# Kernel optimization log

Hardware: AMD Instinct MI355X
Metric: run time of the kernel (lower is better)

The kernel has to match this reference:

```python
import jax, jax.numpy as jnp
import numpy as np

N = 50000      # nodes
E = 600000     # edges
F_IN = 128     # num_node_features
H = 128        # hidden_channels
C = 10         # num_classes
G = 128        # graphs in batch


def setup_inputs() -> dict:
    key = jax.random.key(0)
    ks = jax.random.split(key, 12)
    x = jax.random.normal(ks[0], (N, F_IN), dtype=jnp.float32)
    edge_index = jax.random.randint(ks[1], (2, E), 0, N, dtype=jnp.int64)
    batch = jnp.sort(jax.random.randint(ks[2], (N,), 0, G, dtype=jnp.int64))
    s = 0.05
    return {
        "x": x,
        "W1": jax.random.normal(ks[3], (F_IN, H), jnp.float32) * s,
        "b1": jnp.zeros((H,), jnp.float32),
        "W2": jax.random.normal(ks[4], (H, H), jnp.float32) * s,
        "b2": jnp.zeros((H,), jnp.float32),
        "W3": jax.random.normal(ks[5], (H, H), jnp.float32) * s,
        "b3": jnp.zeros((H,), jnp.float32),
        "Wl": jax.random.normal(ks[6], (H, C), jnp.float32) * s,
        "bl": jnp.zeros((C,), jnp.float32),
        "edge_index": edge_index,
        "batch": batch,
    }


def _gcn_conv(h, W, b, src, dst, norm, n):
    # h: [N, din] -> linear (no bias), gather, scale, scatter-add, + bias
    h = h @ W                                  # [N, dout]
    msg = norm[:, None] * h[src]               # [E+N, dout]
    out = jax.ops.segment_sum(msg, dst, num_segments=n)
    return out + b


def reference(x, W1, b1, W2, b2, W3, b3, Wl, bl, edge_index, batch):
    n = x.shape[0]
    # add self-loops (PyG GCNConv default) and symmetric normalization
    loop = jnp.arange(n, dtype=edge_index.dtype)
    src = jnp.concatenate([edge_index[0], loop])   # [E+N]
    dst = jnp.concatenate([edge_index[1], loop])   # [E+N]
    deg = jax.ops.segment_sum(jnp.ones_like(dst, dtype=x.dtype), dst, num_segments=n)
    dinv = jnp.where(deg > 0, jax.lax.rsqrt(deg), 0.0)
    norm = dinv[src] * dinv[dst]                   # [E+N]

    h = jax.nn.relu(_gcn_conv(x, W1, b1, src, dst, norm, n))
    h = jax.nn.relu(_gcn_conv(h, W2, b2, src, dst, norm, n))
    h = jax.nn.relu(_gcn_conv(h, W3, b3, src, dst, norm, n))

    # global mean pool over graph ids
    sums = jax.ops.segment_sum(h, batch, num_segments=G)           # [G, H]
    cnts = jax.ops.segment_sum(jnp.ones((n,), h.dtype), batch, num_segments=G)
    pooled = sums / jnp.maximum(cnts, 1.0)[:, None]

    # dropout is identity at inference; final linear classifier
    return pooled @ Wl + bl                                        # [G, C]
```

## Files before the change

### kernel.cpp

```cpp
#include <hip/hip_runtime.h>

#define HID 128
#define CLS 10
#define RCAP 64

typedef short short8 __attribute__((ext_vector_type(8)));
typedef float f32x4 __attribute__((ext_vector_type(4)));

__device__ __forceinline__ unsigned short f2bf(float f) {
  union { float f; unsigned u; } v; v.f = f;
  unsigned u = v.u;
  return (unsigned short)((u + 0x7FFFu + ((u >> 16) & 1u)) >> 16);
}
__device__ __forceinline__ float bf_lo(unsigned p) { return __uint_as_float(p << 16); }
__device__ __forceinline__ float bf_hi(unsigned p) { return __uint_as_float(p & 0xFFFF0000u); }


__global__ __launch_bounds__(256) void zero_wt(int* __restrict__ degi, int n, int nbN,
                                               float* __restrict__ pooled, int gh,
                                               const float* __restrict__ W1,
                                               const float* __restrict__ W2,
                                               const float* __restrict__ W3,
                                               unsigned short* __restrict__ Wt) {
  int b = blockIdx.x;
  if (b < nbN) {
    int i = b * 256 + threadIdx.x;
    if (i < n) degi[i] = 0;
    if (i < gh) pooled[i] = 0.f;
    return;
  }
  int wb = b - nbN;
  int mat = wb >> 4;
  int part = wb & 15;
  const float* W = (mat == 0) ? W1 : (mat == 1) ? W2 : W3;
  unsigned short* o = Wt + (size_t)mat * HID * HID;
  int base = part * (HID * HID / 16);
  for (int r = 0; r < HID * HID / 16; r += 256) {
    int idx = base + r + threadIdx.x;
    int k = idx >> 7, nn = idx & 127;
    o[nn * HID + k] = f2bf(W[idx]);
  }
}

__global__ __launch_bounds__(256) void degree_k(const int* __restrict__ dst,
                                                int* __restrict__ degi,
                                                int* __restrict__ eslot, int E) {
  int e = blockIdx.x * 256 + threadIdx.x;
  if (e < E) eslot[e] = atomicAdd(&degi[dst[e]], 1);
}

__global__ __launch_bounds__(256) void csr_fill(const int* __restrict__ src,
                                                const int* __restrict__ dst,
                                                const int* __restrict__ eslot,
                                                int* __restrict__ col_src, int E) {
  int e = blockIdx.x * 256 + threadIdx.x;
  if (e >= E) return;
  int slot = eslot[e];
  if (slot < RCAP) col_src[(size_t)dst[e] * RCAP + slot] = src[e];
}


#define WTP 136

__global__ __launch_bounds__(256) void gemm_mfma(const void* __restrict__ Aptr,
                                                 int a_fp32,
                                                 const unsigned short* __restrict__ Wt,
                                                 const int* __restrict__ degi,
                                                 unsigned short* __restrict__ Tb,
                                                 int nrows) {
  __shared__ unsigned short sW[HID][WTP];
  int tid = threadIdx.x;
  int wave = tid >> 6, lane = tid & 63;
  int m_lo = lane & 15, quad = lane >> 4;
  int row0 = blockIdx.x * 128;
  int rbase = row0 + wave * 32;

  uint4 araw[2][4];
#pragma unroll
  for (int tr = 0; tr < 2; ++tr) {
    int grow = rbase + tr * 16 + m_lo;
    int gr = (grow < nrows) ? grow : (nrows - 1);
    if (a_fp32) {
      const float* Arow = (const float*)Aptr + (size_t)gr * HID;
#pragma unroll
      for (int kb = 0; kb < 4; ++kb) {
        float4 f0 = *(const float4*)&Arow[kb * 32 + quad * 8];
        float4 f1 = *(const float4*)&Arow[kb * 32 + quad * 8 + 4];
        uint4 u;
        u.x = (unsigned)f2bf(f0.x) | ((unsigned)f2bf(f0.y) << 16);
        u.y = (unsigned)f2bf(f0.z) | ((unsigned)f2bf(f0.w) << 16);
        u.z = (unsigned)f2bf(f1.x) | ((unsigned)f2bf(f1.y) << 16);
        u.w = (unsigned)f2bf(f1.z) | ((unsigned)f2bf(f1.w) << 16);
        araw[tr][kb] = u;
      }
    } else {
      const uint4* Arow = (const uint4*)((const unsigned*)Aptr + (size_t)gr * 64);
#pragma unroll
      for (int kb = 0; kb < 4; ++kb) araw[tr][kb] = Arow[kb * 4 + quad];
    }
  }

  const uint4* Wt4 = (const uint4*)Wt;
#pragma unroll
  for (int i = 0; i < 8; ++i) {
    int idx = i * 256 + tid;
    *(uint4*)&sW[idx >> 4][(idx & 15) * 8] = Wt4[idx];
  }
  __syncthreads();

  f32x4 acc[2][8];
#pragma unroll
  for (int tr = 0; tr < 2; ++tr)
#pragma unroll
    for (int tc = 0; tc < 8; ++tc) acc[tr][tc] = (f32x4)(0.f);

#pragma unroll
  for (int kb = 0; kb < 4; ++kb) {
    short8 b[8];
#pragma unroll
    for (int tc = 0; tc < 8; ++tc) {
      union { uint4 u; short8 s; } cv;
      cv.u = *(const uint4*)&sW[tc * 16 + m_lo][kb * 32 + quad * 8];
      b[tc] = cv.s;
    }
#pragma unroll
    for (int tr = 0; tr < 2; ++tr) {
      union { uint4 u; short8 s; } av;
      av.u = araw[tr][kb];
#pragma unroll
      for (int tc = 0; tc < 8; ++tc)
        acc[tr][tc] = __builtin_amdgcn_mfma_f32_16x16x32_bf16(av.s, b[tc], acc[tr][tc], 0, 0, 0);
    }
  }

#pragma unroll
  for (int tr = 0; tr < 2; ++tr) {
#pragma unroll
    for (int r = 0; r < 4; ++r) {
      int grow = rbase + tr * 16 + quad * 4 + r;
      if (grow < nrows) {
        float s = rsqrtf((float)degi[grow] + 1.0f);
        unsigned short* orow = &Tb[(size_t)grow * HID];
#pragma unroll
        for (int tc = 0; tc < 8; ++tc)
          orow[tc * 16 + m_lo] = f2bf(s * acc[tr][tc][r]);
      }
    }
  }
}


__global__ __launch_bounds__(256) void aggregate(const unsigned* __restrict__ Tb2,
                                                 const int* __restrict__ degi,
                                                 const int* __restrict__ col_src,
                                                 const float* __restrict__ bias,
                                                 unsigned* __restrict__ Hb, int n) {
  int w = (blockIdx.x * 256 + threadIdx.x) >> 6;
  int lane = threadIdx.x & 63;
  int sub = lane >> 4;
  int l4 = lane & 15;
  int node = w * 4 + sub;
  if (node >= n) return;

  uint4 sv = *(const uint4*)&Tb2[(size_t)node * 64 + l4 * 4];
  float a0 = bf_lo(sv.x), a1 = bf_hi(sv.x), a2 = bf_lo(sv.y), a3 = bf_hi(sv.y);
  float a4 = bf_lo(sv.z), a5 = bf_hi(sv.z), a6 = bf_lo(sv.w), a7 = bf_hi(sv.w);
  int deg = degi[node];
  const int* row = &col_src[(size_t)node * RCAP];
  int j = 0;
  for (; j + 8 <= deg; j += 8) {
    int idx[8];
#pragma unroll
    for (int u = 0; u < 8; ++u) idx[u] = row[j + u];
    uint4 v[8];
#pragma unroll
    for (int u = 0; u < 8; ++u) v[u] = *(const uint4*)&Tb2[(size_t)idx[u] * 64 + l4 * 4];
#pragma unroll
    for (int u = 0; u < 8; ++u) {
      a0 += bf_lo(v[u].x); a1 += bf_hi(v[u].x);
      a2 += bf_lo(v[u].y); a3 += bf_hi(v[u].y);
      a4 += bf_lo(v[u].z); a5 += bf_hi(v[u].z);
      a6 += bf_lo(v[u].w); a7 += bf_hi(v[u].w);
    }
  }
  if (j + 4 <= deg) {
    int idx[4];
#pragma unroll
    for (int u = 0; u < 4; ++u) idx[u] = row[j + u];
    uint4 v[4];
#pragma unroll
    for (int u = 0; u < 4; ++u) v[u] = *(const uint4*)&Tb2[(size_t)idx[u] * 64 + l4 * 4];
#pragma unroll
    for (int u = 0; u < 4; ++u) {
      a0 += bf_lo(v[u].x); a1 += bf_hi(v[u].x);
      a2 += bf_lo(v[u].y); a3 += bf_hi(v[u].y);
      a4 += bf_lo(v[u].z); a5 += bf_hi(v[u].z);
      a6 += bf_lo(v[u].w); a7 += bf_hi(v[u].w);
    }
    j += 4;
  }
  for (; j < deg; ++j) {
    uint4 v = *(const uint4*)&Tb2[(size_t)row[j] * 64 + l4 * 4];
    a0 += bf_lo(v.x); a1 += bf_hi(v.x);
    a2 += bf_lo(v.y); a3 += bf_hi(v.y);
    a4 += bf_lo(v.z); a5 += bf_hi(v.z);
    a6 += bf_lo(v.w); a7 += bf_hi(v.w);
  }
  float di = rsqrtf((float)deg + 1.0f);
  float4 bs0 = *(const float4*)&bias[l4 * 8];
  float4 bs1 = *(const float4*)&bias[l4 * 8 + 4];
  a0 = fmaxf(di * a0 + bs0.x, 0.f);
  a1 = fmaxf(di * a1 + bs0.y, 0.f);
  a2 = fmaxf(di * a2 + bs0.z, 0.f);
  a3 = fmaxf(di * a3 + bs0.w, 0.f);
  a4 = fmaxf(di * a4 + bs1.x, 0.f);
  a5 = fmaxf(di * a5 + bs1.y, 0.f);
  a6 = fmaxf(di * a6 + bs1.z, 0.f);
  a7 = fmaxf(di * a7 + bs1.w, 0.f);
  uint4 o;
  o.x = (unsigned)f2bf(a0) | ((unsigned)f2bf(a1) << 16);
  o.y = (unsigned)f2bf(a2) | ((unsigned)f2bf(a3) << 16);
  o.z = (unsigned)f2bf(a4) | ((unsigned)f2bf(a5) << 16);
  o.w = (unsigned)f2bf(a6) | ((unsigned)f2bf(a7) << 16);
  *(uint4*)&Hb[(size_t)node * 64 + l4 * 4] = o;
}


__global__ __launch_bounds__(64) void pool_partial(const unsigned* __restrict__ Hb,
                                                   const int* __restrict__ batch,
                                                   float* __restrict__ pooled, int n) {
  int t = threadIdx.x;
  int s = blockIdx.x * 16;
  if (s >= n) return;
  int e = min(s + 16, n);
  int g = batch[s];
  float ax = 0.f, ay = 0.f;
  for (int i = s; i < e; ++i) {
    int bi = batch[i];
    if (bi != g) {
      atomicAdd(&pooled[g * HID + 2 * t], ax);
      atomicAdd(&pooled[g * HID + 2 * t + 1], ay);
      ax = ay = 0.f;
      g = bi;
    }
    unsigned v = Hb[(size_t)i * 64 + t];
    ax += bf_lo(v);
    ay += bf_hi(v);
  }
  atomicAdd(&pooled[g * HID + 2 * t], ax);
  atomicAdd(&pooled[g * HID + 2 * t + 1], ay);
}

__global__ __launch_bounds__(128) void classify_k(const float* __restrict__ pooled,
                                                  const int* __restrict__ batch,
                                                  const float* __restrict__ Wl,
                                                  const float* __restrict__ bl,
                                                  float* __restrict__ out, int n) {
  int g = blockIdx.x;
  int t = threadIdx.x;
  int lo = 0, hi = n;
  while (lo < hi) { int mid = (lo + hi) >> 1; if (batch[mid] < g) lo = mid + 1; else hi = mid; }
  int s = lo;
  hi = n;
  while (lo < hi) { int mid = (lo + hi) >> 1; if (batch[mid] < g + 1) lo = mid + 1; else hi = mid; }
  float c = fmaxf((float)(lo - s), 1.0f);
  __shared__ float p[HID];
  p[t] = pooled[g * HID + t] / c;
  __syncthreads();
  if (t < CLS) {
    float o = bl[t];
    for (int j = 0; j < HID; ++j) o += p[j] * Wl[j * CLS + t];
    out[g * CLS + t] = o;
  }
}


extern "C" void kernel_launch(void* const* d_in, const int* in_sizes, int n_in,
                              void* d_out, int out_size, void* d_ws, size_t ws_size,
                              hipStream_t stream) {
  const float* x  = (const float*)d_in[0];
  const float* W1 = (const float*)d_in[1];
  const float* b1 = (const float*)d_in[2];
  const float* W2 = (const float*)d_in[3];
  const float* b2 = (const float*)d_in[4];
  const float* W3 = (const float*)d_in[5];
  const float* b3 = (const float*)d_in[6];
  const float* Wl = (const float*)d_in[7];
  const float* bl = (const float*)d_in[8];
  const int* edge_index = (const int*)d_in[9];
  const int* batch = (const int*)d_in[10];

  const int N = in_sizes[10];
  const int E = in_sizes[9] / 2;
  const int G = out_size / CLS;
  const int* src = edge_index;
  const int* dst = edge_index + E;

  uintptr_t p = (uintptr_t)d_ws;
  auto take = [&](size_t bytes) -> void* {
    void* r = (void*)p;
    p += (bytes + 255) & ~(size_t)255;
    return r;
  };
  int*      degi      = (int*)take((size_t)N * 4);
  int*      eslot     = (int*)take((size_t)E * 4);
  int*      col_src   = (int*)take((size_t)N * RCAP * 4);
  unsigned short* WtA = (unsigned short*)take((size_t)3 * HID * HID * 2);
  unsigned short* bufTb = (unsigned short*)take((size_t)N * HID * 2);
  unsigned* bufHb     = (unsigned*)take((size_t)N * 64 * 4);
  float*    pooled    = (float*)take((size_t)G * HID * 4);

  int nbN = (N + 255) / 256;
  int nbE = (E + 255) / 256;

  zero_wt<<<nbN + 48, 256, 0, stream>>>(degi, N, nbN, pooled, G * HID, W1, W2, W3, WtA);
  degree_k<<<nbE, 256, 0, stream>>>(dst, degi, eslot, E);
  csr_fill<<<nbE, 256, 0, stream>>>(src, dst, eslot, col_src, E);

  int gemmBlocks = (N + 127) / 128;
  int waves = (N + 3) / 4;
  int aggBlocks = (waves + 3) / 4;

  gemm_mfma<<<gemmBlocks, 256, 0, stream>>>(x, 1, WtA, degi, bufTb, N);
  aggregate<<<aggBlocks, 256, 0, stream>>>((unsigned*)bufTb, degi, col_src, b1, bufHb, N);
  gemm_mfma<<<gemmBlocks, 256, 0, stream>>>(bufHb, 0, WtA + (size_t)HID * HID, degi, bufTb, N);
  aggregate<<<aggBlocks, 256, 0, stream>>>((unsigned*)bufTb, degi, col_src, b2, bufHb, N);
  gemm_mfma<<<gemmBlocks, 256, 0, stream>>>(bufHb, 0, WtA + (size_t)2 * HID * HID, degi, bufTb, N);
  aggregate<<<aggBlocks, 256, 0, stream>>>((unsigned*)bufTb, degi, col_src, b3, bufHb, N);

  pool_partial<<<(N + 15) / 16, 64, 0, stream>>>(bufHb, batch, pooled, N);
  classify_k<<<G, 128, 0, stream>>>(pooled, batch, Wl, bl, (float*)d_out, N);
}
```

Before: 261.1 us.

## Fuse degree/CSR fill kernels and fuse last aggregation with mean-pool

Merges the degree-count and CSR-fill kernels into one pass that writes the column index right after the atomic slot reservation, dropping the eslot buffer and one launch. Fuses the final layer's aggregation with global pooling: each block aggregates 16 nodes into shared memory and then reduces per graph with atomics, skipping the bf16 write and re-read of the last hidden layer. The pooled sums now use fp32 activations instead of bf16-rounded ones, which slightly changes numerics.

```diff
diff --git a/kernel.cpp b/kernel.cpp
--- a/kernel.cpp
+++ b/kernel.cpp
@@ -42,21 +42,15 @@
   }
 }
 
-__global__ __launch_bounds__(256) void degree_k(const int* __restrict__ dst,
-                                                int* __restrict__ degi,
-                                                int* __restrict__ eslot, int E) {
-  int e = blockIdx.x * 256 + threadIdx.x;
-  if (e < E) eslot[e] = atomicAdd(&degi[dst[e]], 1);
-}
-
-__global__ __launch_bounds__(256) void csr_fill(const int* __restrict__ src,
-                                                const int* __restrict__ dst,
-                                                const int* __restrict__ eslot,
-                                                int* __restrict__ col_src, int E) {
+__global__ __launch_bounds__(256) void degree_fill(const int* __restrict__ src,
+                                                   const int* __restrict__ dst,
+                                                   int* __restrict__ degi,
+                                                   int* __restrict__ col_src, int E) {
   int e = blockIdx.x * 256 + threadIdx.x;
   if (e >= E) return;
-  int slot = eslot[e];
-  if (slot < RCAP) col_src[(size_t)dst[e] * RCAP + slot] = src[e];
+  int d = dst[e];
+  int slot = atomicAdd(&degi[d], 1);
+  if (slot < RCAP) col_src[(size_t)d * RCAP + slot] = src[e];
 }
 
 
@@ -150,6 +144,68 @@
 }
 
 
+__device__ __forceinline__ void agg_node(const unsigned* __restrict__ Tb2,
+                                         const int* __restrict__ degi,
+                                         const int* __restrict__ col_src,
+                                         const float* __restrict__ bias,
+                                         int node, int l4, float a[8]) {
+  uint4 sv = *(const uint4*)&Tb2[(size_t)node * 64 + l4 * 4];
+  a[0] = bf_lo(sv.x); a[1] = bf_hi(sv.x); a[2] = bf_lo(sv.y); a[3] = bf_hi(sv.y);
+  a[4] = bf_lo(sv.z); a[5] = bf_hi(sv.z); a[6] = bf_lo(sv.w); a[7] = bf_hi(sv.w);
+  int deg = degi[node];
+  const int* row = &col_src[(size_t)node * RCAP];
+  int j = 0;
+  for (; j + 8 <= deg; j += 8) {
+    int idx[8];
+#pragma unroll
+    for (int u = 0; u < 8; ++u) idx[u] = row[j + u];
+    uint4 v[8];
+#pragma unroll
+    for (int u = 0; u < 8; ++u) v[u] = *(const uint4*)&Tb2[(size_t)idx[u] * 64 + l4 * 4];
+#pragma unroll
+    for (int u = 0; u < 8; ++u) {
+      a[0] += bf_lo(v[u].x); a[1] += bf_hi(v[u].x);
+      a[2] += bf_lo(v[u].y); a[3] += bf_hi(v[u].y);
+      a[4] += bf_lo(v[u].z); a[5] += bf_hi(v[u].z);
+      a[6] += bf_lo(v[u].w); a[7] += bf_hi(v[u].w);
+    }
+  }
+  if (j + 4 <= deg) {
+    int idx[4];
+#pragma unroll
+    for (int u = 0; u < 4; ++u) idx[u] = row[j + u];
+    uint4 v[4];
+#pragma unroll
+    for (int u = 0; u < 4; ++u) v[u] = *(const uint4*)&Tb2[(size_t)idx[u] * 64 + l4 * 4];
+#pragma unroll
+    for (int u = 0; u < 4; ++u) {
+      a[0] += bf_lo(v[u].x); a[1] += bf_hi(v[u].x);
+      a[2] += bf_lo(v[u].y); a[3] += bf_hi(v[u].y);
+      a[4] += bf_lo(v[u].z); a[5] += bf_hi(v[u].z);
+      a[6] += bf_lo(v[u].w); a[7] += bf_hi(v[u].w);
+    }
+    j += 4;
+  }
+  for (; j < deg; ++j) {
+    uint4 v = *(const uint4*)&Tb2[(size_t)row[j] * 64 + l4 * 4];
+    a[0] += bf_lo(v.x); a[1] += bf_hi(v.x);
+    a[2] += bf_lo(v.y); a[3] += bf_hi(v.y);
+    a[4] += bf_lo(v.z); a[5] += bf_hi(v.z);
+    a[6] += bf_lo(v.w); a[7] += bf_hi(v.w);
+  }
+  float di = rsqrtf((float)deg + 1.0f);
+  float4 bs0 = *(const float4*)&bias[l4 * 8];
+  float4 bs1 = *(const float4*)&bias[l4 * 8 + 4];
+  a[0] = fmaxf(di * a[0] + bs0.x, 0.f);
+  a[1] = fmaxf(di * a[1] + bs0.y, 0.f);
+  a[2] = fmaxf(di * a[2] + bs0.z, 0.f);
+  a[3] = fmaxf(di * a[3] + bs0.w, 0.f);
+  a[4] = fmaxf(di * a[4] + bs1.x, 0.f);
+  a[5] = fmaxf(di * a[5] + bs1.y, 0.f);
+  a[6] = fmaxf(di * a[6] + bs1.z, 0.f);
+  a[7] = fmaxf(di * a[7] + bs1.w, 0.f);
+}
+
 __global__ __launch_bounds__(256) void aggregate(const unsigned* __restrict__ Tb2,
                                                  const int* __restrict__ degi,
                                                  const int* __restrict__ col_src,
@@ -161,94 +217,56 @@
   int l4 = lane & 15;
   int node = w * 4 + sub;
   if (node >= n) return;
-
-  uint4 sv = *(const uint4*)&Tb2[(size_t)node * 64 + l4 * 4];
-  float a0 = bf_lo(sv.x), a1 = bf_hi(sv.x), a2 = bf_lo(sv.y), a3 = bf_hi(sv.y);
-  float a4 = bf_lo(sv.z), a5 = bf_hi(sv.z), a6 = bf_lo(sv.w), a7 = bf_hi(sv.w);
-  int deg = degi[node];
-  const int* row = &col_src[(size_t)node * RCAP];
-  int j = 0;
-  for (; j + 8 <= deg; j += 8) {
-    int idx[8];
-#pragma unroll
-    for (int u = 0; u < 8; ++u) idx[u] = row[j + u];
-    uint4 v[8];
-#pragma unroll
-    for (int u = 0; u < 8; ++u) v[u] = *(const uint4*)&Tb2[(size_t)idx[u] * 64 + l4 * 4];
-#pragma unroll
-    for (int u = 0; u < 8; ++u) {
-      a0 += bf_lo(v[u].x); a1 += bf_hi(v[u].x);
-      a2 += bf_lo(v[u].y); a3 += bf_hi(v[u].y);
-      a4 += bf_lo(v[u].z); a5 += bf_hi(v[u].z);
-      a6 += bf_lo(v[u].w); a7 += bf_hi(v[u].w);
-    }
-  }
-  if (j + 4 <= deg) {
-    int idx[4];
-#pragma unroll
-    for (int u = 0; u < 4; ++u) idx[u] = row[j + u];
-    uint4 v[4];
-#pragma unroll
-    for (int u = 0; u < 4; ++u) v[u] = *(const uint4*)&Tb2[(size_t)idx[u] * 64 + l4 * 4];
-#pragma unroll
-    for (int u = 0; u < 4; ++u) {
-      a0 += bf_lo(v[u].x); a1 += bf_hi(v[u].x);
-      a2 += bf_lo(v[u].y); a3 += bf_hi(v[u].y);
-      a4 += bf_lo(v[u].z); a5 += bf_hi(v[u].z);
-      a6 += bf_lo(v[u].w); a7 += bf_hi(v[u].w);
-    }
-    j += 4;
-  }
-  for (; j < deg; ++j) {
-    uint4 v = *(const uint4*)&Tb2[(size_t)row[j] * 64 + l4 * 4];
-    a0 += bf_lo(v.x); a1 += bf_hi(v.x);
-    a2 += bf_lo(v.y); a3 += bf_hi(v.y);
-    a4 += bf_lo(v.z); a5 += bf_hi(v.z);
-    a6 += bf_lo(v.w); a7 += bf_hi(v.w);
-  }
-  float di = rsqrtf((float)deg + 1.0f);
-  float4 bs0 = *(const float4*)&bias[l4 * 8];
-  float4 bs1 = *(const float4*)&bias[l4 * 8 + 4];
-  a0 = fmaxf(di * a0 + bs0.x, 0.f);
-  a1 = fmaxf(di * a1 + bs0.y, 0.f);
-  a2 = fmaxf(di * a2 + bs0.z, 0.f);
-  a3 = fmaxf(di * a3 + bs0.w, 0.f);
-  a4 = fmaxf(di * a4 + bs1.x, 0.f);
-  a5 = fmaxf(di * a5 + bs1.y, 0.f);
-  a6 = fmaxf(di * a6 + bs1.z, 0.f);
-  a7 = fmaxf(di * a7 + bs1.w, 0.f);
+  float a[8];
+  agg_node(Tb2, degi, col_src, bias, node, l4, a);
   uint4 o;
-  o.x = (unsigned)f2bf(a0) | ((unsigned)f2bf(a1) << 16);
-  o.y = (unsigned)f2bf(a2) | ((unsigned)f2bf(a3) << 16);
-  o.z = (unsigned)f2bf(a4) | ((unsigned)f2bf(a5) << 16);
-  o.w = (unsigned)f2bf(a6) | ((unsigned)f2bf(a7) << 16);
+  o.x = (unsigned)f2bf(a[0]) | ((unsigned)f2bf(a[1]) << 16);
+  o.y = (unsigned)f2bf(a[2]) | ((unsigned)f2bf(a[3]) << 16);
+  o.z = (unsigned)f2bf(a[4]) | ((unsigned)f2bf(a[5]) << 16);
+  o.w = (unsigned)f2bf(a[6]) | ((unsigned)f2bf(a[7]) << 16);
   *(uint4*)&Hb[(size_t)node * 64 + l4 * 4] = o;
 }
 
-
-__global__ __launch_bounds__(64) void pool_partial(const unsigned* __restrict__ Hb,
-                                                   const int* __restrict__ batch,
-                                                   float* __restrict__ pooled, int n) {
-  int t = threadIdx.x;
-  int s = blockIdx.x * 16;
-  if (s >= n) return;
-  int e = min(s + 16, n);
-  int g = batch[s];
-  float ax = 0.f, ay = 0.f;
-  for (int i = s; i < e; ++i) {
-    int bi = batch[i];
-    if (bi != g) {
-      atomicAdd(&pooled[g * HID + 2 * t], ax);
-      atomicAdd(&pooled[g * HID + 2 * t + 1], ay);
-      ax = ay = 0.f;
-      g = bi;
-    }
-    unsigned v = Hb[(size_t)i * 64 + t];
-    ax += bf_lo(v);
-    ay += bf_hi(v);
-  }
-  atomicAdd(&pooled[g * HID + 2 * t], ax);
-  atomicAdd(&pooled[g * HID + 2 * t + 1], ay);
+#define SPP 132
+
+__global__ __launch_bounds__(256) void aggregate_pool(const unsigned* __restrict__ Tb2,
+                                                      const int* __restrict__ degi,
+                                                      const int* __restrict__ col_src,
+                                                      const float* __restrict__ bias,
+                                                      const int* __restrict__ batch,
+                                                      float* __restrict__ pooled, int n) {
+  __shared__ float sP[16][SPP];
+  int tid = threadIdx.x;
+  int wave = tid >> 6, lane = tid & 63;
+  int sub = lane >> 4;
+  int l4 = lane & 15;
+  int base = blockIdx.x * 16;
+  int nl = wave * 4 + sub;
+  int node = base + nl;
+  bool active = (node < n);
+
+  float a[8] = {0.f, 0.f, 0.f, 0.f, 0.f, 0.f, 0.f, 0.f};
+  if (active) agg_node(Tb2, degi, col_src, bias, node, l4, a);
+  *(float4*)&sP[nl][l4 * 8] = make_float4(a[0], a[1], a[2], a[3]);
+  *(float4*)&sP[nl][l4 * 8 + 4] = make_float4(a[4], a[5], a[6], a[7]);
+  __syncthreads();
+
+  if (tid < HID) {
+    int g = -1;
+    float acc = 0.f;
+    for (int i = 0; i < 16; ++i) {
+      int nd = base + i;
+      if (nd >= n) break;
+      int bi = batch[nd];
+      if (bi != g) {
+        if (g >= 0) atomicAdd(&pooled[g * HID + tid], acc);
+        acc = 0.f;
+        g = bi;
+      }
+      acc += sP[i][tid];
+    }
+    if (g >= 0) atomicAdd(&pooled[g * HID + tid], acc);
+  }
 }
 
 __global__ __launch_bounds__(128) void classify_k(const float* __restrict__ pooled,
@@ -303,7 +321,6 @@
     return r;
   };
   int*      degi      = (int*)take((size_t)N * 4);
-  int*      eslot     = (int*)take((size_t)E * 4);
   int*      col_src   = (int*)take((size_t)N * RCAP * 4);
   unsigned short* WtA = (unsigned short*)take((size_t)3 * HID * HID * 2);
   unsigned short* bufTb = (unsigned short*)take((size_t)N * HID * 2);
@@ -314,8 +331,7 @@
   int nbE = (E + 255) / 256;
 
   zero_wt<<<nbN + 48, 256, 0, stream>>>(degi, N, nbN, pooled, G * HID, W1, W2, W3, WtA);
-  degree_k<<<nbE, 256, 0, stream>>>(dst, degi, eslot, E);
-  csr_fill<<<nbE, 256, 0, stream>>>(src, dst, eslot, col_src, E);
+  degree_fill<<<nbE, 256, 0, stream>>>(src, dst, degi, col_src, E);
 
   int gemmBlocks = (N + 127) / 128;
   int waves = (N + 3) / 4;
@@ -326,8 +342,7 @@
   gemm_mfma<<<gemmBlocks, 256, 0, stream>>>(bufHb, 0, WtA + (size_t)HID * HID, degi, bufTb, N);
   aggregate<<<aggBlocks, 256, 0, stream>>>((unsigned*)bufTb, degi, col_src, b2, bufHb, N);
   gemm_mfma<<<gemmBlocks, 256, 0, stream>>>(bufHb, 0, WtA + (size_t)2 * HID * HID, degi, bufTb, N);
-  aggregate<<<aggBlocks, 256, 0, stream>>>((unsigned*)bufTb, degi, col_src, b3, bufHb, N);
-
-  pool_partial<<<(N + 15) / 16, 64, 0, stream>>>(bufHb, batch, pooled, N);
+  aggregate_pool<<<(N + 15) / 16, 256, 0, stream>>>((unsigned*)bufTb, degi, col_src, b3,
+                                                    batch, pooled, N);
   classify_k<<<G, 128, 0, stream>>>(pooled, batch, Wl, bl, (float*)d_out, N);
 }
```

After: 250.0 us (median of 2 runs). 4.2% less time.
